# Optimization experiments

Measured on AMD Instinct MI355X. Metric: run time of the kernel, lower is better.

Reference implementation:

```python
import jax, jax.numpy as jnp
import numpy as np

MASK_FILL = -(2 ** 15)  # value used by the torch module's masked_fill


def setup_inputs() -> dict:
    key = jax.random.key(0)
    kq, kk, kv, km = jax.random.split(key, 4)
    B, H, S, D = 2, 16, 2048, 64
    Q = jax.random.normal(kq, (B, H, S, D), dtype=jnp.float32)
    K = jax.random.normal(kk, (B, H, S, D), dtype=jnp.float32)
    V = jax.random.normal(kv, (B, H, S, D), dtype=jnp.float32)
    mask = jax.random.randint(km, (B, 1, S, S), 0, 2, dtype=jnp.int32)
    return {"Q": Q, "K": K, "V": V, "mask": mask}


def reference(Q, K, V, mask):
    d_k = Q.shape[-1]
    # scores: [B,H,S,S]
    e = jnp.einsum('bhqd,bhkd->bhqk', Q, K) / jnp.sqrt(jnp.float32(d_k)).astype(Q.dtype)
    e = jnp.where(mask == 0, jnp.asarray(MASK_FILL, dtype=e.dtype), e)
    a = jax.nn.softmax(e, axis=-1)
    y = jnp.einsum('bhqk,bhkd->bhqd', a, V)
    return y
```

## Files before the change

kernel.cpp:

```cpp
#include <hip/hip_runtime.h>
#include <stdint.h>


#define SS 2048
#define DD 64
#define KT 32
#define NT 64
#define QB 64

#define KS_OFF 0
#define VT_OFF 4608
#define PS_OFF 9728
#define SMEM_SZ 14848

#define SCL2 0.18033688011112042f

typedef __attribute__((ext_vector_type(8))) short bf16x8;
typedef __attribute__((ext_vector_type(4))) float f32x4;

static __device__ __forceinline__ uint16_t f2bf(float f) {
  return (uint16_t)((__float_as_uint(f) + 0x8000u) >> 16);
}
static __device__ __forceinline__ unsigned pk2(float f0, float f1) {
  uint32_t a = __float_as_uint(f1) + 0x8000u;
  uint32_t b = __float_as_uint(f0) + 0x8000u;
  return __builtin_amdgcn_perm(a, b, 0x07060302u);
}

__global__ __launch_bounds__(256, 2)
void attn_mfma(const float* __restrict__ Q, const float* __restrict__ K,
               const float* __restrict__ V, const int* __restrict__ mask,
               float* __restrict__ out) {
  __shared__ alignas(16) uint8_t smem[SMEM_SZ];

  const int tid = threadIdx.x;
  const int wv = tid >> 6;
  const int l = tid & 63;
  const int n16 = l & 15;
  const int quad = l >> 4;

  const int bid = blockIdx.x;
  const int qblk = bid & 31;
  const int bh = bid >> 5;
  const int b = bh >> 4;
  const size_t base = (size_t)bh * SS * DD;
  const int qglob = qblk * QB + 16 * wv + n16;

  const int sr = tid >> 3;
  const int sd = (tid & 7) * 8;
  const int vxor = 8 * (tid & 3);

  bf16x8 qf[2];
#pragma unroll
  for (int kd = 0; kd < 2; ++kd) {
    const float* qp = Q + base + (size_t)qglob * DD + kd * 32 + quad * 8;
    float4 qa = *(const float4*)(qp);
    float4 qb = *(const float4*)(qp + 4);
    uint4 pk;
    pk.x = pk2(qa.x, qa.y); pk.y = pk2(qa.z, qa.w);
    pk.z = pk2(qb.x, qb.y); pk.w = pk2(qb.z, qb.w);
    qf[kd] = __builtin_bit_cast(bf16x8, pk);
  }

  f32x4 oaccT[4];
#pragma unroll
  for (int dg = 0; dg < 4; ++dg)
#pragma unroll
    for (int r = 0; r < 4; ++r) oaccT[dg][r] = 0.f;
  float lrun = 0.f;

  float4 ka, kb, va, vb;
  {
    const float* kp = K + base + (size_t)sr * DD + sd;
    const float* vp = V + base + (size_t)sr * DD + sd;
    ka = *(const float4*)(kp); kb = *(const float4*)(kp + 4);
    va = *(const float4*)(vp); vb = *(const float4*)(vp + 4);
  }

  const int* mbase = mask + (size_t)b * SS * SS + (size_t)qglob * SS;
  uint8_t* prow = smem + PS_OFF + wv * 1280 + n16 * 80;

  for (int t = 0; t < NT; ++t) {
    __syncthreads();

    {
      uint4 kw;
      kw.x = pk2(ka.x, ka.y); kw.y = pk2(ka.z, ka.w);
      kw.z = pk2(kb.x, kb.y); kw.w = pk2(kb.z, kb.w);
      *(uint4*)(smem + KS_OFF + sr * 144 + sd * 2) = kw;
      uint16_t* vt = (uint16_t*)(smem + VT_OFF);
      const int kx = sr ^ vxor;
      vt[(sd + 0) * 40 + kx] = f2bf(va.x);
      vt[(sd + 1) * 40 + kx] = f2bf(va.y);
      vt[(sd + 2) * 40 + kx] = f2bf(va.z);
      vt[(sd + 3) * 40 + kx] = f2bf(va.w);
      vt[(sd + 4) * 40 + kx] = f2bf(vb.x);
      vt[(sd + 5) * 40 + kx] = f2bf(vb.y);
      vt[(sd + 6) * 40 + kx] = f2bf(vb.z);
      vt[(sd + 7) * 40 + kx] = f2bf(vb.w);
    }
    __syncthreads();

    if (t + 1 < NT) {
      const float* kp = K + base + (size_t)((t + 1) * KT + sr) * DD + sd;
      const float* vp = V + base + (size_t)((t + 1) * KT + sr) * DD + sd;
      ka = *(const float4*)(kp); kb = *(const float4*)(kp + 4);
      va = *(const float4*)(vp); vb = *(const float4*)(vp + 4);
    }

    f32x4 sacc[2];
#pragma unroll
    for (int kg = 0; kg < 2; ++kg) {
#pragma unroll
      for (int r = 0; r < 4; ++r) sacc[kg][r] = 0.f;
      const uint8_t* krow = smem + KS_OFF + (kg * 16 + n16) * 144;
#pragma unroll
      for (int kd = 0; kd < 2; ++kd) {
        bf16x8 kf = *(const bf16x8*)(krow + kd * 64 + quad * 16);
        sacc[kg] = __builtin_amdgcn_mfma_f32_16x16x32_bf16(kf, qf[kd], sacc[kg], 0, 0, 0);
      }
    }

    const int* mrow = mbase + t * KT;
    float lt = 0.f;
#pragma unroll
    for (int kg = 0; kg < 2; ++kg) {
      int4 mi = *(const int4*)(mrow + kg * 16 + quad * 4);
      float p0 = (mi.x != 0) ? __builtin_amdgcn_exp2f(sacc[kg][0] * SCL2) : 0.f;
      float p1 = (mi.y != 0) ? __builtin_amdgcn_exp2f(sacc[kg][1] * SCL2) : 0.f;
      float p2 = (mi.z != 0) ? __builtin_amdgcn_exp2f(sacc[kg][2] * SCL2) : 0.f;
      float p3 = (mi.w != 0) ? __builtin_amdgcn_exp2f(sacc[kg][3] * SCL2) : 0.f;
      lt += (p0 + p1) + (p2 + p3);
      uint2 pw;
      pw.x = pk2(p0, p1);
      pw.y = pk2(p2, p3);
      *(uint2*)(prow + kg * 32 + quad * 8) = pw;
    }
    lt += __shfl_xor(lt, 16);
    lt += __shfl_xor(lt, 32);
    lrun += lt;

    __builtin_amdgcn_s_waitcnt(0xC07F);
    asm volatile("" ::: "memory");

    bf16x8 pf = *(const bf16x8*)(prow + quad * 16);
#pragma unroll
    for (int dg = 0; dg < 4; ++dg) {
      const int d = 16 * dg + n16;
      const int ch = quad ^ ((d >> 3) & 3);
      bf16x8 vf = *(const bf16x8*)(smem + VT_OFF + d * 80 + ch * 16);
      oaccT[dg] = __builtin_amdgcn_mfma_f32_16x16x32_bf16(vf, pf, oaccT[dg], 0, 0, 0);
    }
  }

  const float inv = (lrun > 0.f) ? (1.f / lrun) : 0.f;
  float* orow = out + base + (size_t)qglob * DD;
#pragma unroll
  for (int dg = 0; dg < 4; ++dg) {
    float4 o;
    o.x = oaccT[dg][0] * inv;
    o.y = oaccT[dg][1] * inv;
    o.z = oaccT[dg][2] * inv;
    o.w = oaccT[dg][3] * inv;
    *(float4*)(orow + 16 * dg + 4 * quad) = o;
  }
}

extern "C" void kernel_launch(void* const* d_in, const int* in_sizes, int n_in,
                              void* d_out, int out_size, void* d_ws, size_t ws_size,
                              hipStream_t stream) {
  (void)in_sizes; (void)n_in; (void)out_size; (void)d_ws; (void)ws_size;
  const float* Q = (const float*)d_in[0];
  const float* K = (const float*)d_in[1];
  const float* V = (const float*)d_in[2];
  const int* mask = (const int*)d_in[3];
  float* out = (float*)d_out;
  attn_mfma<<<1024, 256, 0, stream>>>(Q, K, V, mask, out);
}
```

Baseline: 211.9 us.

## Double-buffer K/V LDS tiles, prefetch two tiles ahead, and prefetch mask

Splits the K and transposed-V LDS areas into two buffers, so each iteration writes tile t+1 while computing on tile t, with one barrier per iteration instead of two. Global loads of K/V now run two tiles ahead, and the mask row for the next tile is loaded one iteration early. The V transpose store now writes packed 32-bit pairs instead of single bf16 stores. LDS use grows and more registers stay live, which could affect occupancy at two blocks per CU.

```diff
diff --git a/kernel.cpp b/kernel.cpp
--- a/kernel.cpp
+++ b/kernel.cpp
@@ -8,24 +8,30 @@
 #define NT 64
 #define QB 64
 
-#define KS_OFF 0
-#define VT_OFF 4608
-#define PS_OFF 9728
-#define SMEM_SZ 14848
+#define KS0 0
+#define KS1 4608
+#define VT0 9216
+#define VT1 14336
+#define PS_OFF 19456
+#define SMEM_SZ 24576
 
 #define SCL2 0.18033688011112042f
 
 typedef __attribute__((ext_vector_type(8))) short bf16x8;
 typedef __attribute__((ext_vector_type(4))) float f32x4;
 
-static __device__ __forceinline__ uint16_t f2bf(float f) {
-  return (uint16_t)((__float_as_uint(f) + 0x8000u) >> 16);
-}
 static __device__ __forceinline__ unsigned pk2(float f0, float f1) {
   uint32_t a = __float_as_uint(f1) + 0x8000u;
   uint32_t b = __float_as_uint(f0) + 0x8000u;
   return __builtin_amdgcn_perm(a, b, 0x07060302u);
 }
+
+#define BAR() do {                              \
+  asm volatile("" ::: "memory");                \
+  __builtin_amdgcn_s_waitcnt(0xC07F);           \
+  __builtin_amdgcn_s_barrier();                 \
+  asm volatile("" ::: "memory");                \
+} while (0)
 
 __global__ __launch_bounds__(256, 2)
 void attn_mfma(const float* __restrict__ Q, const float* __restrict__ K,
@@ -48,7 +54,9 @@
 
   const int sr = tid >> 3;
   const int sd = (tid & 7) * 8;
-  const int vxor = 8 * (tid & 3);
+  const int vk = (tid >> 4) * 2;
+  const int vd = (tid & 15) * 4;
+  const int vkx = vk ^ (8 * ((vd >> 3) & 3));
 
   bf16x8 qf[2];
 #pragma unroll
@@ -72,48 +80,71 @@
   float4 ka, kb, va, vb;
   {
     const float* kp = K + base + (size_t)sr * DD + sd;
-    const float* vp = V + base + (size_t)sr * DD + sd;
     ka = *(const float4*)(kp); kb = *(const float4*)(kp + 4);
-    va = *(const float4*)(vp); vb = *(const float4*)(vp + 4);
-  }
-
+    const float* vp = V + base + (size_t)vk * DD + vd;
+    va = *(const float4*)(vp); vb = *(const float4*)(vp + DD);
+  }
+  {
+    uint4 kw;
+    kw.x = pk2(ka.x, ka.y); kw.y = pk2(ka.z, ka.w);
+    kw.z = pk2(kb.x, kb.y); kw.w = pk2(kb.z, kb.w);
+    *(uint4*)(smem + KS0 + sr * 144 + sd * 2) = kw;
+    uint16_t* vt = (uint16_t*)(smem + VT0);
+    *(uint32_t*)(vt + (vd + 0) * 40 + vkx) = pk2(va.x, vb.x);
+    *(uint32_t*)(vt + (vd + 1) * 40 + vkx) = pk2(va.y, vb.y);
+    *(uint32_t*)(vt + (vd + 2) * 40 + vkx) = pk2(va.z, vb.z);
+    *(uint32_t*)(vt + (vd + 3) * 40 + vkx) = pk2(va.w, vb.w);
+  }
+  {
+    const float* kp = K + base + (size_t)(KT + sr) * DD + sd;
+    ka = *(const float4*)(kp); kb = *(const float4*)(kp + 4);
+    const float* vp = V + base + (size_t)(KT + vk) * DD + vd;
+    va = *(const float4*)(vp); vb = *(const float4*)(vp + DD);
+  }
   const int* mbase = mask + (size_t)b * SS * SS + (size_t)qglob * SS;
+  int4 mi0 = *(const int4*)(mbase + quad * 4);
+  int4 mi1 = *(const int4*)(mbase + 16 + quad * 4);
+
   uint8_t* prow = smem + PS_OFF + wv * 1280 + n16 * 80;
 
+  BAR();
+
   for (int t = 0; t < NT; ++t) {
-    __syncthreads();
+    const int db = t & 1;
+    const int ksc = db ? KS1 : KS0;
+    const int vtc = db ? VT1 : VT0;
+    const int ksn = db ? KS0 : KS1;
+    const int vtn = db ? VT0 : VT1;
 
     {
       uint4 kw;
       kw.x = pk2(ka.x, ka.y); kw.y = pk2(ka.z, ka.w);
       kw.z = pk2(kb.x, kb.y); kw.w = pk2(kb.z, kb.w);
-      *(uint4*)(smem + KS_OFF + sr * 144 + sd * 2) = kw;
-      uint16_t* vt = (uint16_t*)(smem + VT_OFF);
-      const int kx = sr ^ vxor;
-      vt[(sd + 0) * 40 + kx] = f2bf(va.x);
-      vt[(sd + 1) * 40 + kx] = f2bf(va.y);
-      vt[(sd + 2) * 40 + kx] = f2bf(va.z);
-      vt[(sd + 3) * 40 + kx] = f2bf(va.w);
-      vt[(sd + 4) * 40 + kx] = f2bf(vb.x);
-      vt[(sd + 5) * 40 + kx] = f2bf(vb.y);
-      vt[(sd + 6) * 40 + kx] = f2bf(vb.z);
-      vt[(sd + 7) * 40 + kx] = f2bf(vb.w);
-    }
-    __syncthreads();
-
-    if (t + 1 < NT) {
-      const float* kp = K + base + (size_t)((t + 1) * KT + sr) * DD + sd;
-      const float* vp = V + base + (size_t)((t + 1) * KT + sr) * DD + sd;
+      *(uint4*)(smem + ksn + sr * 144 + sd * 2) = kw;
+      uint16_t* vt = (uint16_t*)(smem + vtn);
+      *(uint32_t*)(vt + (vd + 0) * 40 + vkx) = pk2(va.x, vb.x);
+      *(uint32_t*)(vt + (vd + 1) * 40 + vkx) = pk2(va.y, vb.y);
+      *(uint32_t*)(vt + (vd + 2) * 40 + vkx) = pk2(va.z, vb.z);
+      *(uint32_t*)(vt + (vd + 3) * 40 + vkx) = pk2(va.w, vb.w);
+    }
+
+    {
+      const int tp2 = (t + 2 < NT) ? (t + 2) : (NT - 1);
+      const float* kp = K + base + (size_t)(tp2 * KT + sr) * DD + sd;
+      const float* vp = V + base + (size_t)(tp2 * KT + vk) * DD + vd;
       ka = *(const float4*)(kp); kb = *(const float4*)(kp + 4);
-      va = *(const float4*)(vp); vb = *(const float4*)(vp + 4);
-    }
+      va = *(const float4*)(vp); vb = *(const float4*)(vp + DD);
+    }
+    const int tp1 = (t + 1 < NT) ? (t + 1) : (NT - 1);
+    int4 mn0 = *(const int4*)(mbase + tp1 * KT + quad * 4);
+    int4 mn1 = *(const int4*)(mbase + tp1 * KT + 16 + quad * 4);
 
     f32x4 sacc[2];
 #pragma unroll
     for (int kg = 0; kg < 2; ++kg) {
 #pragma unroll
       for (int r = 0; r < 4; ++r) sacc[kg][r] = 0.f;
-      const uint8_t* krow = smem + KS_OFF + (kg * 16 + n16) * 144;
+      const uint8_t* krow = smem + ksc + (kg * 16 + n16) * 144;
 #pragma unroll
       for (int kd = 0; kd < 2; ++kd) {
         bf16x8 kf = *(const bf16x8*)(krow + kd * 64 + quad * 16);
@@ -121,20 +152,28 @@
       }
     }
 
-    const int* mrow = mbase + t * KT;
     float lt = 0.f;
-#pragma unroll
-    for (int kg = 0; kg < 2; ++kg) {
-      int4 mi = *(const int4*)(mrow + kg * 16 + quad * 4);
-      float p0 = (mi.x != 0) ? __builtin_amdgcn_exp2f(sacc[kg][0] * SCL2) : 0.f;
-      float p1 = (mi.y != 0) ? __builtin_amdgcn_exp2f(sacc[kg][1] * SCL2) : 0.f;
-      float p2 = (mi.z != 0) ? __builtin_amdgcn_exp2f(sacc[kg][2] * SCL2) : 0.f;
-      float p3 = (mi.w != 0) ? __builtin_amdgcn_exp2f(sacc[kg][3] * SCL2) : 0.f;
+    {
+      float p0 = (mi0.x != 0) ? __builtin_amdgcn_exp2f(sacc[0][0] * SCL2) : 0.f;
+      float p1 = (mi0.y != 0) ? __builtin_amdgcn_exp2f(sacc[0][1] * SCL2) : 0.f;
+      float p2 = (mi0.z != 0) ? __builtin_amdgcn_exp2f(sacc[0][2] * SCL2) : 0.f;
+      float p3 = (mi0.w != 0) ? __builtin_amdgcn_exp2f(sacc[0][3] * SCL2) : 0.f;
       lt += (p0 + p1) + (p2 + p3);
       uint2 pw;
       pw.x = pk2(p0, p1);
       pw.y = pk2(p2, p3);
-      *(uint2*)(prow + kg * 32 + quad * 8) = pw;
+      *(uint2*)(prow + quad * 8) = pw;
+    }
+    {
+      float p0 = (mi1.x != 0) ? __builtin_amdgcn_exp2f(sacc[1][0] * SCL2) : 0.f;
+      float p1 = (mi1.y != 0) ? __builtin_amdgcn_exp2f(sacc[1][1] * SCL2) : 0.f;
+      float p2 = (mi1.z != 0) ? __builtin_amdgcn_exp2f(sacc[1][2] * SCL2) : 0.f;
+      float p3 = (mi1.w != 0) ? __builtin_amdgcn_exp2f(sacc[1][3] * SCL2) : 0.f;
+      lt += (p0 + p1) + (p2 + p3);
+      uint2 pw;
+      pw.x = pk2(p0, p1);
+      pw.y = pk2(p2, p3);
+      *(uint2*)(prow + 32 + quad * 8) = pw;
     }
     lt += __shfl_xor(lt, 16);
     lt += __shfl_xor(lt, 32);
@@ -148,9 +187,13 @@
     for (int dg = 0; dg < 4; ++dg) {
       const int d = 16 * dg + n16;
       const int ch = quad ^ ((d >> 3) & 3);
-      bf16x8 vf = *(const bf16x8*)(smem + VT_OFF + d * 80 + ch * 16);
+      bf16x8 vf = *(const bf16x8*)(smem + vtc + d * 80 + ch * 16);
       oaccT[dg] = __builtin_amdgcn_mfma_f32_16x16x32_bf16(vf, pf, oaccT[dg], 0, 0, 0);
     }
+
+    mi0 = mn0; mi1 = mn1;
+
+    BAR();
   }
 
   const float inv = (lrun > 0.f) ? (1.f / lrun) : 0.f;
```

Measured after the change: 197.1 us. 7.0% less time.

## Double-buffer K/V tiles in LDS with 64-key tiles and XOR swizzle

Applied to the files above, without the earlier changes.

Doubles the key tile to 64, double-buffers K and transposed V in shared memory so there is one barrier per iteration, and prefetches global K/V two tiles ahead. Adds XOR swizzling for the K, V and P layouts in place of padding, uses the hardware packed bf16 convert instruction, and raises launch bounds to 4 blocks per CU. The aim is to hide global load latency and cut barrier and conversion overhead. In exchange it uses more LDS (40KB) and more registers for the prefetch, which could limit occupancy.

```diff
diff --git a/kernel.cpp b/kernel.cpp
--- a/kernel.cpp
+++ b/kernel.cpp
@@ -4,30 +4,38 @@
 
 #define SS 2048
 #define DD 64
-#define KT 32
-#define NT 64
+#define KT 64
+#define NT 32
 #define QB 64
 
-#define KS_OFF 0
-#define VT_OFF 4608
-#define PS_OFF 9728
-#define SMEM_SZ 14848
+#define KS0 0
+#define KS1 8192
+#define VT0 16384
+#define VT1 24576
+#define PS_OFF 32768
+#define SMEM_SZ 40960
 
 #define SCL2 0.18033688011112042f
 
 typedef __attribute__((ext_vector_type(8))) short bf16x8;
 typedef __attribute__((ext_vector_type(4))) float f32x4;
 
-static __device__ __forceinline__ uint16_t f2bf(float f) {
-  return (uint16_t)((__float_as_uint(f) + 0x8000u) >> 16);
+static __device__ __forceinline__ unsigned pk2(float f0, float f1) {
+  unsigned r;
+  asm("v_cvt_pk_bf16_f32 %0, %1, %2" : "=v"(r) : "v"(f0), "v"(f1));
+  return r;
 }
-static __device__ __forceinline__ unsigned pk2(float f0, float f1) {
-  uint32_t a = __float_as_uint(f1) + 0x8000u;
-  uint32_t b = __float_as_uint(f0) + 0x8000u;
-  return __builtin_amdgcn_perm(a, b, 0x07060302u);
-}
-
-__global__ __launch_bounds__(256, 2)
+
+#define BAR() do {                              \
+  asm volatile("" ::: "memory");                \
+  __builtin_amdgcn_s_waitcnt(0xC07F);           \
+  __builtin_amdgcn_s_barrier();                 \
+  asm volatile("" ::: "memory");                \
+} while (0)
+
+#define MFMA(A, B, C) __builtin_amdgcn_mfma_f32_16x16x32_bf16((A), (B), (C), 0, 0, 0)
+
+__global__ __launch_bounds__(256, 4)
 void attn_mfma(const float* __restrict__ Q, const float* __restrict__ K,
                const float* __restrict__ V, const int* __restrict__ mask,
                float* __restrict__ out) {
@@ -38,6 +46,7 @@
   const int l = tid & 63;
   const int n16 = l & 15;
   const int quad = l >> 4;
+  const int xr = (n16 & 7) << 4;
 
   const int bid = blockIdx.x;
   const int qblk = bid & 31;
@@ -46,86 +55,115 @@
   const size_t base = (size_t)bh * SS * DD;
   const int qglob = qblk * QB + 16 * wv + n16;
 
-  const int sr = tid >> 3;
-  const int sd = (tid & 7) * 8;
-  const int vxor = 8 * (tid & 3);
-
-  bf16x8 qf[2];
-#pragma unroll
-  for (int kd = 0; kd < 2; ++kd) {
-    const float* qp = Q + base + (size_t)qglob * DD + kd * 32 + quad * 8;
+  const int kr = tid >> 4;
+  const int kc = tid & 15;
+  const int kxr = (kr & 7) << 4;
+  const int vk = (tid & 15) << 2;
+  const int vdb = (tid >> 4) << 2;
+
+  bf16x8 qf0, qf1;
+  {
+    const float* qp = Q + base + (size_t)qglob * DD + quad * 8;
     float4 qa = *(const float4*)(qp);
     float4 qb = *(const float4*)(qp + 4);
     uint4 pk;
     pk.x = pk2(qa.x, qa.y); pk.y = pk2(qa.z, qa.w);
     pk.z = pk2(qb.x, qb.y); pk.w = pk2(qb.z, qb.w);
-    qf[kd] = __builtin_bit_cast(bf16x8, pk);
+    qf0 = __builtin_bit_cast(bf16x8, pk);
+    qa = *(const float4*)(qp + 32);
+    qb = *(const float4*)(qp + 36);
+    pk.x = pk2(qa.x, qa.y); pk.y = pk2(qa.z, qa.w);
+    pk.z = pk2(qb.x, qb.y); pk.w = pk2(qb.z, qb.w);
+    qf1 = __builtin_bit_cast(bf16x8, pk);
   }
 
-  f32x4 oaccT[4];
+  f32x4 oacc[4];
 #pragma unroll
   for (int dg = 0; dg < 4; ++dg)
 #pragma unroll
-    for (int r = 0; r < 4; ++r) oaccT[dg][r] = 0.f;
+    for (int r = 0; r < 4; ++r) oacc[dg][r] = 0.f;
   float lrun = 0.f;
 
-  float4 ka, kb, va, vb;
-  {
-    const float* kp = K + base + (size_t)sr * DD + sd;
-    const float* vp = V + base + (size_t)sr * DD + sd;
-    ka = *(const float4*)(kp); kb = *(const float4*)(kp + 4);
-    va = *(const float4*)(vp); vb = *(const float4*)(vp + 4);
-  }
+  float4 kA0, kA1, kA2, kA3, vA0, vA1, vA2, vA3;
+
+#define LOADKV(T) do {                                                   \
+    const float* kp_ = K + base + (size_t)((T)*KT + kr) * DD + kc * 4;   \
+    kA0 = *(const float4*)(kp_);                                         \
+    kA1 = *(const float4*)(kp_ + 16 * DD);                               \
+    kA2 = *(const float4*)(kp_ + 32 * DD);                               \
+    kA3 = *(const float4*)(kp_ + 48 * DD);                               \
+    const float* vp_ = V + base + (size_t)((T)*KT + vk) * DD + vdb;      \
+    vA0 = *(const float4*)(vp_);                                         \
+    vA1 = *(const float4*)(vp_ + DD);                                    \
+    vA2 = *(const float4*)(vp_ + 2 * DD);                                \
+    vA3 = *(const float4*)(vp_ + 3 * DD);                                \
+  } while (0)
+
+#define STAGE(KB, VB) do {                                               \
+    uint2 w_;                                                            \
+    w_.x = pk2(kA0.x, kA0.y); w_.y = pk2(kA0.z, kA0.w);                  \
+    *(uint2*)((KB) + (kr) * 128 + ((kc * 8) ^ kxr)) = w_;                \
+    w_.x = pk2(kA1.x, kA1.y); w_.y = pk2(kA1.z, kA1.w);                  \
+    *(uint2*)((KB) + (16 + kr) * 128 + ((kc * 8) ^ kxr)) = w_;           \
+    w_.x = pk2(kA2.x, kA2.y); w_.y = pk2(kA2.z, kA2.w);                  \
+    *(uint2*)((KB) + (32 + kr) * 128 + ((kc * 8) ^ kxr)) = w_;           \
+    w_.x = pk2(kA3.x, kA3.y); w_.y = pk2(kA3.z, kA3.w);                  \
+    *(uint2*)((KB) + (48 + kr) * 128 + ((kc * 8) ^ kxr)) = w_;           \
+    w_.x = pk2(vA0.x, vA1.x); w_.y = pk2(vA2.x, vA3.x);                  \
+    *(uint2*)((VB) + (vdb + 0) * 128 + ((vk * 2) ^ ((((vdb + 0) & 7)) << 4))) = w_; \
+    w_.x = pk2(vA0.y, vA1.y); w_.y = pk2(vA2.y, vA3.y);                  \
+    *(uint2*)((VB) + (vdb + 1) * 128 + ((vk * 2) ^ ((((vdb + 1) & 7)) << 4))) = w_; \
+    w_.x = pk2(vA0.z, vA1.z); w_.y = pk2(vA2.z, vA3.z);                  \
+    *(uint2*)((VB) + (vdb + 2) * 128 + ((vk * 2) ^ ((((vdb + 2) & 7)) << 4))) = w_; \
+    w_.x = pk2(vA0.w, vA1.w); w_.y = pk2(vA2.w, vA3.w);                  \
+    *(uint2*)((VB) + (vdb + 3) * 128 + ((vk * 2) ^ ((((vdb + 3) & 7)) << 4))) = w_; \
+  } while (0)
+
+  LOADKV(0);
+  STAGE(smem + KS0, smem + VT0);
+  LOADKV(1);
 
   const int* mbase = mask + (size_t)b * SS * SS + (size_t)qglob * SS;
-  uint8_t* prow = smem + PS_OFF + wv * 1280 + n16 * 80;
+  uint8_t* prow = smem + PS_OFF + wv * 2048 + n16 * 128;
+
+  BAR();
 
   for (int t = 0; t < NT; ++t) {
-    __syncthreads();
+    const int db = t & 1;
+    uint8_t* kbc = smem + (db ? KS1 : KS0);
+    uint8_t* vbc = smem + (db ? VT1 : VT0);
+    uint8_t* kbn = smem + (db ? KS0 : KS1);
+    uint8_t* vbn = smem + (db ? VT0 : VT1);
+
+    const int* mrow = mbase + t * KT;
+    int4 mi0 = *(const int4*)(mrow + 0 * 16 + quad * 4);
+    int4 mi1 = *(const int4*)(mrow + 1 * 16 + quad * 4);
+    int4 mi2 = *(const int4*)(mrow + 2 * 16 + quad * 4);
+    int4 mi3 = *(const int4*)(mrow + 3 * 16 + quad * 4);
+
+    STAGE(kbn, vbn);
 
     {
-      uint4 kw;
-      kw.x = pk2(ka.x, ka.y); kw.y = pk2(ka.z, ka.w);
-      kw.z = pk2(kb.x, kb.y); kw.w = pk2(kb.z, kb.w);
-      *(uint4*)(smem + KS_OFF + sr * 144 + sd * 2) = kw;
-      uint16_t* vt = (uint16_t*)(smem + VT_OFF);
-      const int kx = sr ^ vxor;
-      vt[(sd + 0) * 40 + kx] = f2bf(va.x);
-      vt[(sd + 1) * 40 + kx] = f2bf(va.y);
-      vt[(sd + 2) * 40 + kx] = f2bf(va.z);
-      vt[(sd + 3) * 40 + kx] = f2bf(va.w);
-      vt[(sd + 4) * 40 + kx] = f2bf(vb.x);
-      vt[(sd + 5) * 40 + kx] = f2bf(vb.y);
-      vt[(sd + 6) * 40 + kx] = f2bf(vb.z);
-      vt[(sd + 7) * 40 + kx] = f2bf(vb.w);
-    }
-    __syncthreads();
-
-    if (t + 1 < NT) {
-      const float* kp = K + base + (size_t)((t + 1) * KT + sr) * DD + sd;
-      const float* vp = V + base + (size_t)((t + 1) * KT + sr) * DD + sd;
-      ka = *(const float4*)(kp); kb = *(const float4*)(kp + 4);
-      va = *(const float4*)(vp); vb = *(const float4*)(vp + 4);
-    }
-
-    f32x4 sacc[2];
-#pragma unroll
-    for (int kg = 0; kg < 2; ++kg) {
+      const int tp2 = (t + 2 < NT) ? (t + 2) : (NT - 1);
+      LOADKV(tp2);
+    }
+
+    f32x4 sacc[4];
+#pragma unroll
+    for (int kg = 0; kg < 4; ++kg) {
 #pragma unroll
       for (int r = 0; r < 4; ++r) sacc[kg][r] = 0.f;
-      const uint8_t* krow = smem + KS_OFF + (kg * 16 + n16) * 144;
-#pragma unroll
-      for (int kd = 0; kd < 2; ++kd) {
-        bf16x8 kf = *(const bf16x8*)(krow + kd * 64 + quad * 16);
-        sacc[kg] = __builtin_amdgcn_mfma_f32_16x16x32_bf16(kf, qf[kd], sacc[kg], 0, 0, 0);
-      }
-    }
-
-    const int* mrow = mbase + t * KT;
+      const uint8_t* krow = kbc + (kg * 16 + n16) * 128;
+      bf16x8 kf0 = *(const bf16x8*)(krow + ((quad * 16) ^ xr));
+      bf16x8 kf1 = *(const bf16x8*)(krow + ((64 + quad * 16) ^ xr));
+      sacc[kg] = MFMA(kf0, qf0, sacc[kg]);
+      sacc[kg] = MFMA(kf1, qf1, sacc[kg]);
+    }
+
     float lt = 0.f;
 #pragma unroll
-    for (int kg = 0; kg < 2; ++kg) {
-      int4 mi = *(const int4*)(mrow + kg * 16 + quad * 4);
+    for (int kg = 0; kg < 4; ++kg) {
+      int4 mi = (kg == 0) ? mi0 : (kg == 1) ? mi1 : (kg == 2) ? mi2 : mi3;
       float p0 = (mi.x != 0) ? __builtin_amdgcn_exp2f(sacc[kg][0] * SCL2) : 0.f;
       float p1 = (mi.y != 0) ? __builtin_amdgcn_exp2f(sacc[kg][1] * SCL2) : 0.f;
       float p2 = (mi.z != 0) ? __builtin_amdgcn_exp2f(sacc[kg][2] * SCL2) : 0.f;
@@ -134,7 +172,7 @@
       uint2 pw;
       pw.x = pk2(p0, p1);
       pw.y = pk2(p2, p3);
-      *(uint2*)(prow + kg * 32 + quad * 8) = pw;
+      *(uint2*)(prow + ((kg * 32 + quad * 8) ^ xr)) = pw;
     }
     lt += __shfl_xor(lt, 16);
     lt += __shfl_xor(lt, 32);
@@ -143,14 +181,18 @@
     __builtin_amdgcn_s_waitcnt(0xC07F);
     asm volatile("" ::: "memory");
 
-    bf16x8 pf = *(const bf16x8*)(prow + quad * 16);
+    bf16x8 pf0 = *(const bf16x8*)(prow + ((quad * 16) ^ xr));
+    bf16x8 pf1 = *(const bf16x8*)(prow + ((64 + quad * 16) ^ xr));
 #pragma unroll
     for (int dg = 0; dg < 4; ++dg) {
-      const int d = 16 * dg + n16;
-      const int ch = quad ^ ((d >> 3) & 3);
-      bf16x8 vf = *(const bf16x8*)(smem + VT_OFF + d * 80 + ch * 16);
-      oaccT[dg] = __builtin_amdgcn_mfma_f32_16x16x32_bf16(vf, pf, oaccT[dg], 0, 0, 0);
-    }
+      const uint8_t* vrow = vbc + (dg * 16 + n16) * 128;
+      bf16x8 vf0 = *(const bf16x8*)(vrow + ((quad * 16) ^ xr));
+      oacc[dg] = MFMA(vf0, pf0, oacc[dg]);
+      bf16x8 vf1 = *(const bf16x8*)(vrow + ((64 + quad * 16) ^ xr));
+      oacc[dg] = MFMA(vf1, pf1, oacc[dg]);
+    }
+
+    BAR();
   }
 
   const float inv = (lrun > 0.f) ? (1.f / lrun) : 0.f;
@@ -158,10 +200,10 @@
 #pragma unroll
   for (int dg = 0; dg < 4; ++dg) {
     float4 o;
-    o.x = oaccT[dg][0] * inv;
-    o.y = oaccT[dg][1] * inv;
-    o.z = oaccT[dg][2] * inv;
-    o.w = oaccT[dg][3] * inv;
+    o.x = oacc[dg][0] * inv;
+    o.y = oacc[dg][1] * inv;
+    o.z = oacc[dg][2] * inv;
+    o.w = oacc[dg][3] * inv;
     *(float4*)(orow + 16 * dg + 4 * quad) = o;
   }
 }
```

Result: slower. 246.7 us (+16.4%).
